# Optimization experiments

Measured on AMD Instinct MI355X. Metric: run time of the kernel, lower is better.

The kernel has to match this reference:

```python
import jax, jax.numpy as jnp
import numpy as np
from jax import lax

DIM = 2048
N_HEADS = 16
N_KV = 4
HEAD_DIM = DIM // N_HEADS  # 128
ROPE_BASE = 10000.0
SEQ = 4096
BSZ = 1


def bitlinear(x, W):
    # per-row abs-mean scale (detached), ternary round/clamp, straight-through blend
    s = lax.stop_gradient(jnp.clip(jnp.mean(jnp.abs(W), axis=1, keepdims=True), 1e-5, None))
    wt = jnp.clip(jnp.round(W / s), -1.0, 1.0)
    w = lax.stop_gradient(wt - W) + W  # straight-through
    return x @ (w * s).T


def rms_norm(x):
    eps = jnp.finfo(x.dtype).eps
    return x * lax.rsqrt(jnp.mean(x * x, axis=-1, keepdims=True) + eps)


def rope(x, cos, sin):
    half = x.shape[-1] // 2
    x1, x2 = x[..., :half], x[..., half:]
    return jnp.concatenate((x1 * cos + x2 * sin, -x1 * sin + x2 * cos), axis=-1)


def setup_inputs() -> dict:
    key = jax.random.key(0)
    ks = jax.random.split(key, 6)
    kv_dim = N_KV * HEAD_DIM
    return {
        "x": jax.random.normal(ks[0], (BSZ, SEQ, DIM), dtype=jnp.float32),
        "wq": jax.random.normal(ks[1], (DIM, DIM), dtype=jnp.float32) * 0.02,
        "wk": jax.random.normal(ks[2], (kv_dim, DIM), dtype=jnp.float32) * 0.02,
        "wv": jax.random.normal(ks[3], (kv_dim, DIM), dtype=jnp.float32) * 0.02,
        "wp": jax.random.normal(ks[4], (DIM, DIM), dtype=jnp.float32) * 0.02,
        "q_gain": jnp.ones((N_HEADS,), dtype=jnp.float32),
    }


def reference(x, wq, wk, wv, wp, q_gain):
    b, s, d = x.shape
    q = bitlinear(x, wq).reshape(b, s, N_HEADS, HEAD_DIM).transpose(0, 2, 1, 3)  # bhsd
    k = bitlinear(x, wk).reshape(b, s, N_KV, HEAD_DIM).transpose(0, 2, 1, 3)
    v = bitlinear(x, wv).reshape(b, s, N_KV, HEAD_DIM).transpose(0, 2, 1, 3)

    q = rms_norm(q)
    k = rms_norm(k)

    inv_freq = 1.0 / ROPE_BASE ** (jnp.arange(0, HEAD_DIM, 2, dtype=jnp.float32) / HEAD_DIM)
    t = jnp.arange(s, dtype=jnp.float32)
    freqs = jnp.outer(t, inv_freq)  # [s, hd/2]
    cos = jnp.cos(freqs)[None, None].astype(q.dtype)
    sin = jnp.sin(freqs)[None, None].astype(q.dtype)
    q = rope(q, cos, sin)
    k = rope(k, cos, sin)

    q = q * q_gain.astype(q.dtype)[None, :, None, None]

    groups = N_HEADS // N_KV
    k = jnp.repeat(k, groups, axis=1)  # GQA expand to [b, H, s, hd]
    v = jnp.repeat(v, groups, axis=1)

    scale = 1.0 / np.sqrt(HEAD_DIM)
    scores = jnp.einsum("bhqd,bhkd->bhqk", q, k) * scale
    causal = jnp.tril(jnp.ones((s, s), dtype=bool))
    scores = jnp.where(causal[None, None], scores, jnp.finfo(scores.dtype).min)
    attn = jax.nn.softmax(scores, axis=-1)
    y = jnp.einsum("bhqk,bhkd->bhqd", attn, v)

    y = y.transpose(0, 2, 1, 3).reshape(b, s, d)
    return bitlinear(y, wp)
```

## Files before the change

kernel.cpp:

```cpp
#include <hip/hip_runtime.h>
#include <math.h>

typedef unsigned short u16;
typedef short s16x8 __attribute__((ext_vector_type(8)));
typedef short s16x4 __attribute__((ext_vector_type(4)));
typedef float f32x4 __attribute__((ext_vector_type(4)));
typedef u16 u16x4 __attribute__((ext_vector_type(4)));

static constexpr size_t OFF_XB   = 0;
static constexpr size_t OFF_WQKV = 16777216;
static constexpr size_t OFF_KH   = 16777216;
static constexpr size_t OFF_VT   = 20971520;
static constexpr size_t OFF_ML   = 25165824;
static constexpr size_t OFF_WP   = 29360128;
static constexpr size_t OFF_QKV  = 37748736;
static constexpr size_t OFF_Y    = 79691776;

__device__ __forceinline__ u16 f2bf(float f) {
  union { float f; unsigned u; } v; v.f = f;
  unsigned r = v.u + 0x7fffu + ((v.u >> 16) & 1u);
  return (u16)(r >> 16);
}

__device__ __forceinline__ float bf2f(u16 b) {
  union { unsigned u; float f; } v; v.u = ((unsigned)b) << 16;
  return v.f;
}

__device__ __forceinline__ void async16(const u16* g, u16* lds) {
  __builtin_amdgcn_global_load_lds(
      (const __attribute__((address_space(1))) void*)g,
      (__attribute__((address_space(3))) void*)lds, 16, 0, 0);
}

__global__ __launch_bounds__(256) void quant_rows(const float* __restrict__ W,
                                                  u16* __restrict__ out) {
  const int row = blockIdx.x, tid = threadIdx.x;
  const float* src = W + (size_t)row * 2048 + tid * 8;
  float4 a = *(const float4*)(src);
  float4 b = *(const float4*)(src + 4);
  float asum = fabsf(a.x)+fabsf(a.y)+fabsf(a.z)+fabsf(a.w)
             + fabsf(b.x)+fabsf(b.y)+fabsf(b.z)+fabsf(b.w);
  #pragma unroll
  for (int off = 1; off < 64; off <<= 1) asum += __shfl_xor(asum, off, 64);
  __shared__ float red[4];
  if ((tid & 63) == 0) red[tid >> 6] = asum;
  __syncthreads();
  float s = fmaxf((red[0]+red[1]+red[2]+red[3]) * (1.0f/2048.0f), 1e-5f);
  float v[8] = {a.x,a.y,a.z,a.w,b.x,b.y,b.z,b.w};
  u16* dst = out + (size_t)row * 2048 + tid * 8;
  #pragma unroll
  for (int i = 0; i < 8; i++) {
    float q = rintf(v[i] / s);
    q = fminf(fmaxf(q, -1.f), 1.f);
    dst[i] = f2bf(q * s);
  }
}

__global__ __launch_bounds__(256) void cvt_bf16(const float* __restrict__ in,
                                                u16* __restrict__ out) {
  size_t i = ((size_t)blockIdx.x * 256 + threadIdx.x) * 4;
  float4 v = *(const float4*)(in + i);
  u16x4 o;
  o.x = f2bf(v.x); o.y = f2bf(v.y); o.z = f2bf(v.z); o.w = f2bf(v.w);
  *(u16x4*)(out + i) = o;
}

__global__ __launch_bounds__(256) void gemm_bt(const u16* __restrict__ A,
                                               const u16* __restrict__ B,
                                               float* __restrict__ C,
                                               int M, int N, int K) {
  __shared__ u16 sA[128 * 32];
  __shared__ u16 sB[128 * 32];
  const int tid = threadIdx.x;
  const int lane = tid & 63;
  const int wid = tid >> 6;
  const int lr = lane & 15, lq = lane >> 4;
  const int wm = (wid >> 1) * 64, wn = (wid & 1) * 64;
  const size_t m0 = (size_t)blockIdx.y * 128, n0 = (size_t)blockIdx.x * 128;

  const int r0 = tid >> 2, c0 = (tid & 3) * 8;
  const u16* Ab0 = A + (m0 + r0) * (size_t)K + c0;
  const u16* Ab1 = A + (m0 + 64 + r0) * (size_t)K + c0;
  const u16* Bb0 = B + (n0 + r0) * (size_t)K + c0;
  const u16* Bb1 = B + (n0 + 64 + r0) * (size_t)K + c0;
  u16* sA0 = &sA[tid * 8];
  u16* sA1 = &sA[(256 + tid) * 8];
  u16* sB0 = &sB[tid * 8];
  u16* sB1 = &sB[(256 + tid) * 8];

  f32x4 acc[4][4] = {};

  for (int kt = 0; kt < K; kt += 32) {
    async16(Ab0 + kt, sA0);
    async16(Ab1 + kt, sA1);
    async16(Bb0 + kt, sB0);
    async16(Bb1 + kt, sB1);
    __syncthreads();
    s16x8 af[4], bf[4];
    #pragma unroll
    for (int mt = 0; mt < 4; mt++)
      af[mt] = *(const s16x8*)&sA[(wm + mt * 16 + lr) * 32 + lq * 8];
    #pragma unroll
    for (int nt = 0; nt < 4; nt++)
      bf[nt] = *(const s16x8*)&sB[(wn + nt * 16 + lr) * 32 + lq * 8];
    #pragma unroll
    for (int mt = 0; mt < 4; mt++)
      #pragma unroll
      for (int nt = 0; nt < 4; nt++)
        acc[mt][nt] = __builtin_amdgcn_mfma_f32_16x16x32_bf16(af[mt], bf[nt], acc[mt][nt], 0, 0, 0);
    __syncthreads();
  }
  #pragma unroll
  for (int mt = 0; mt < 4; mt++)
    #pragma unroll
    for (int nt = 0; nt < 4; nt++)
      #pragma unroll
      for (int r = 0; r < 4; r++) {
        size_t m = m0 + wm + mt * 16 + lq * 4 + r;
        size_t n = n0 + wn + nt * 16 + lr;
        C[m * (size_t)N + n] = acc[mt][nt][r];
      }
}

__global__ __launch_bounds__(256) void prep_qk(const float* __restrict__ qkv,
                                               const float* __restrict__ qgain,
                                               u16* __restrict__ Qh,
                                               u16* __restrict__ Kh) {
  const int s = blockIdx.y;
  const int j = blockIdx.x * 4 + (threadIdx.x >> 6);
  const int t = threadIdx.x & 63;
  const float* row = qkv + (size_t)s * 3072 + (size_t)j * 128;
  float x1 = row[t], x2 = row[t + 64];
  float ss = x1 * x1 + x2 * x2;
  #pragma unroll
  for (int off = 1; off < 64; off <<= 1) ss += __shfl_xor(ss, off, 64);
  float rn = rsqrtf(ss * (1.0f / 128.0f) + 1.1920929e-07f);
  float invf = exp2f(-(float)t * 0.20762050593048096f);
  float ang = (float)s * invf;
  float sn, c;
  sincosf(ang, &sn, &c);
  if (j < 16) {
    float g = qgain[j] * 0.12751738f;
    float q1 = x1 * rn, q2 = x2 * rn;
    float o1 = (q1 * c + q2 * sn) * g;
    float o2 = (-q1 * sn + q2 * c) * g;
    u16* dst = Qh + ((size_t)j * 4096 + s) * 128;
    dst[t] = f2bf(o1); dst[t + 64] = f2bf(o2);
  } else {
    float k1 = x1 * rn, k2 = x2 * rn;
    float o1 = k1 * c + k2 * sn;
    float o2 = -k1 * sn + k2 * c;
    u16* dst = Kh + ((size_t)(j - 16) * 4096 + s) * 128;
    dst[t] = f2bf(o1); dst[t + 64] = f2bf(o2);
  }
}

__global__ __launch_bounds__(256) void vtrans(const float* __restrict__ qkv,
                                              u16* __restrict__ Vtg) {
  __shared__ float tile[64][67];
  const int tid = threadIdx.x;
  const int s0 = blockIdx.y * 64;
  const int c0 = blockIdx.x * 64;
  #pragma unroll
  for (int it = 0; it < 4; it++) {
    int i = it * 256 + tid;
    int r = i >> 4, c = (i & 15) * 4;
    float4 v = *(const float4*)(qkv + (size_t)(s0 + r) * 3072 + 2560 + c0 + c);
    tile[r][c] = v.x; tile[r][c + 1] = v.y; tile[r][c + 2] = v.z; tile[r][c + 3] = v.w;
  }
  __syncthreads();
  #pragma unroll
  for (int it = 0; it < 2; it++) {
    int i = it * 256 + tid;
    int dl = i >> 3, sc = (i & 7) * 8;
    s16x8 ov;
    #pragma unroll
    for (int jj = 0; jj < 8; jj++) ov[jj] = (short)f2bf(tile[sc + jj][dl]);
    *(s16x8*)&Vtg[(size_t)(c0 + dl) * 4096 + s0 + sc] = ov;
  }
}

#define SEG(qt,a,b,s) ((unsigned)((qt)|((a)<<5)|((b)<<11)|((s)<<18)))
__constant__ unsigned SEGTAB[128] = {
  SEG(0,0,2,127),   SEG(15,0,15,14),
  SEG(15,15,32,15), 0,
  SEG(1,0,4,127),   SEG(14,0,13,12),
  SEG(14,13,30,13), 0,
  SEG(2,0,6,127),   SEG(13,0,11,10),
  SEG(13,11,28,11), 0,
  SEG(3,0,8,127),   SEG(12,0,9,8),
  SEG(12,9,26,9),   0,
  SEG(4,0,10,127),  SEG(11,0,7,6),
  SEG(11,7,24,7),   0,
  SEG(5,0,12,127),  SEG(10,0,5,4),
  SEG(10,5,22,5),   0,
  SEG(6,0,14,127),  SEG(9,0,3,2),
  SEG(9,3,20,3),    0,
  SEG(7,0,16,127),  SEG(8,0,1,0),
  SEG(8,1,18,1),    0,
  SEG(16,0,16,16),  0,
  SEG(16,16,33,17), 0,
  SEG(16,33,34,18), SEG(17,0,15,19),
  SEG(17,15,31,20), 0,
  SEG(17,31,36,21), SEG(18,0,12,22),
  SEG(18,12,28,23), 0,
  SEG(18,28,38,24), SEG(19,0,6,25),
  SEG(19,6,23,26),  0,
  SEG(19,23,39,27), 0,
  SEG(19,39,40,28), SEG(20,0,15,29),
  SEG(20,15,32,30), 0,
  SEG(20,32,42,31), SEG(21,0,6,32),
  SEG(21,6,22,33),  0,
  SEG(21,22,39,34), 0,
  SEG(21,39,44,35), SEG(22,0,11,36),
  SEG(22,11,27,37), 0,
  SEG(22,27,44,38), 0,
  SEG(22,44,46,39), SEG(23,0,14,40),
  SEG(23,14,30,41), 0,
  SEG(23,30,47,42), 0,
  SEG(23,47,48,43), SEG(24,0,15,44),
  SEG(24,15,31,45), 0,
  SEG(24,31,48,46), 0,
  SEG(24,48,50,47), SEG(25,0,14,48),
  SEG(25,14,30,49), 0,
  SEG(25,30,47,50), 0,
  SEG(25,47,52,51), SEG(26,0,11,52),
  SEG(26,11,27,53), 0,
  SEG(26,27,44,54), 0,
  SEG(26,44,54,55), SEG(27,0,6,56),
  SEG(27,6,22,57),  0,
  SEG(27,22,39,58), 0,
  SEG(27,39,55,59), 0,
  SEG(27,55,56,60), SEG(28,0,15,61),
  SEG(28,15,32,62), 0,
  SEG(28,32,48,63), 0,
  SEG(28,48,58,64), SEG(29,0,6,65),
  SEG(29,6,23,66),  0,
  SEG(29,23,39,67), 0,
  SEG(29,39,55,68), 0,
  SEG(29,55,60,69), SEG(30,0,12,70),
  SEG(30,12,28,71), 0,
  SEG(30,28,44,72), 0,
  SEG(30,44,61,73), 0,
  SEG(30,61,62,74), SEG(31,0,15,75),
  SEG(31,15,31,76), 0,
  SEG(31,31,48,77), 0,
  SEG(31,48,64,78), 0,
};
__constant__ unsigned char CBASE[24] = {0,2,4,6,8,10,12,14, 16,19,22,25,29,32,36,40, 44,48,52,56,61,65,70,75};
__constant__ unsigned char CCNT[24]  = {2,2,2,2,2,2,2,2, 3,3,3,4,3,4,4,4, 4,4,4,5,4,5,5,4};

__global__ __launch_bounds__(256, 2) void attn(const u16* __restrict__ Q,
                                               const u16* __restrict__ Kh,
                                               const u16* __restrict__ Vt,
                                               u16* __restrict__ Y,
                                               u16* __restrict__ Opart,
                                               float* __restrict__ MLpart) {
  const int tid = threadIdx.x, lane = tid & 63, wid = tid >> 6;
  const int lr = lane & 15, lq = lane >> 4;
  const int b = blockIdx.x;
  const int h = b & 15, unit = b >> 4;
  const int kvh = h >> 2;

  __shared__ u16 sK[64][136];
  __shared__ u16 sVt[128][72];

  const u16* Kbase = Kh + (size_t)kvh * 4096 * 128;
  const u16* Vbase = Vt + (size_t)kvh * 128 * 4096;

  #pragma unroll 1
  for (int si = 0; si < 2; ++si) {
    const unsigned sd = SEGTAB[unit * 2 + si];
    const int qt = sd & 31;
    const int t0 = (sd >> 5) & 63;
    const int t1 = (sd >> 11) & 127;
    const int slot = (sd >> 18) & 127;
    if (t1 <= t0) continue;
    const int qbase = qt * 128;

    s16x8 qf[2][4];
    #pragma unroll
    for (int f = 0; f < 2; f++) {
      const u16* qp = Q + ((size_t)h * 4096 + qbase + wid * 32 + f * 16 + lr) * 128 + lq * 8;
      #pragma unroll
      for (int kc = 0; kc < 4; kc++) qf[f][kc] = *(const s16x8*)(qp + kc * 32);
    }

    f32x4 oacc[2][8] = {};
    float mrow[2] = {-1e30f, -1e30f};
    float lrow[2] = {0.f, 0.f};

    for (int t = t0; t < t1; ++t) {
      #pragma unroll
      for (int it = 0; it < 4; it++) {
        int idx = it * 256 + tid;
        int kr = idx >> 4, kc8 = (idx & 15) * 8;
        *(s16x8*)&sK[kr][kc8] = *(const s16x8*)(Kbase + (size_t)(t * 64 + kr) * 128 + kc8);
      }
      #pragma unroll
      for (int it = 0; it < 4; it++) {
        int idx = it * 256 + tid;
        int vd = idx >> 3, vc = (idx & 7) * 8;
        s16x8 v = *(const s16x8*)(Vbase + (size_t)vd * 4096 + t * 64 + vc);
        int g0 = ((vc >> 2) & 3) * 16 + (vc >> 4) * 4;
        int g1 = (((vc >> 2) & 3) + 1) * 16 + (vc >> 4) * 4;
        s16x4 lo = {v[0], v[1], v[2], v[3]};
        s16x4 hi = {v[4], v[5], v[6], v[7]};
        *(s16x4*)&sVt[vd][g0] = lo;
        *(s16x4*)&sVt[vd][g1] = hi;
      }
      __syncthreads();

      f32x4 sacc[2][4] = {};
      #pragma unroll
      for (int nt = 0; nt < 4; nt++)
        #pragma unroll
        for (int kc = 0; kc < 4; kc++) {
          s16x8 kf = *(const s16x8*)&sK[nt * 16 + lr][kc * 32 + lq * 8];
          sacc[0][nt] = __builtin_amdgcn_mfma_f32_16x16x32_bf16(kf, qf[0][kc], sacc[0][nt], 0, 0, 0);
          sacc[1][nt] = __builtin_amdgcn_mfma_f32_16x16x32_bf16(kf, qf[1][kc], sacc[1][nt], 0, 0, 0);
        }

      if (t >= 2 * qt) {
        #pragma unroll
        for (int f = 0; f < 2; f++) {
          int qg = qbase + wid * 32 + f * 16 + lr;
          #pragma unroll
          for (int nt = 0; nt < 4; nt++) {
            int kv0 = t * 64 + nt * 16 + lq * 4;
            #pragma unroll
            for (int r = 0; r < 4; r++)
              if (kv0 + r > qg) sacc[f][nt][r] = -1e30f;
          }
        }
      }

      float mx[2];
      #pragma unroll
      for (int f = 0; f < 2; f++) {
        float m01 = fmaxf(fmaxf(sacc[f][0][0], sacc[f][0][1]), fmaxf(sacc[f][0][2], sacc[f][0][3]));
        float m23 = fmaxf(fmaxf(sacc[f][1][0], sacc[f][1][1]), fmaxf(sacc[f][1][2], sacc[f][1][3]));
        float m45 = fmaxf(fmaxf(sacc[f][2][0], sacc[f][2][1]), fmaxf(sacc[f][2][2], sacc[f][2][3]));
        float m67 = fmaxf(fmaxf(sacc[f][3][0], sacc[f][3][1]), fmaxf(sacc[f][3][2], sacc[f][3][3]));
        mx[f] = fmaxf(fmaxf(m01, m23), fmaxf(m45, m67));
        mx[f] = fmaxf(mx[f], __shfl_xor(mx[f], 16, 64));
        mx[f] = fmaxf(mx[f], __shfl_xor(mx[f], 32, 64));
      }

      bool grow = (mx[0] > mrow[0]) || (mx[1] > mrow[1]);
      if (__any(grow)) {
        #pragma unroll
        for (int f = 0; f < 2; f++) {
          float mn = fmaxf(mrow[f], mx[f]);
          float al = exp2f(mrow[f] - mn);
          mrow[f] = mn;
          lrow[f] *= al;
          #pragma unroll
          for (int dt = 0; dt < 8; dt++)
            #pragma unroll
            for (int r = 0; r < 4; r++) oacc[f][dt][r] *= al;
        }
      }

      s16x4 pf[2][4];
      float rsum[2] = {0.f, 0.f};
      #pragma unroll
      for (int f = 0; f < 2; f++)
        #pragma unroll
        for (int nt = 0; nt < 4; nt++)
          #pragma unroll
          for (int r = 0; r < 4; r++) {
            union { float fv; unsigned u; } pu;
            pu.fv = exp2f(sacc[f][nt][r] - mrow[f]);
            rsum[f] += pu.fv;
            pf[f][nt][r] = (short)(pu.u >> 16);
          }
      #pragma unroll
      for (int f = 0; f < 2; f++) {
        rsum[f] += __shfl_xor(rsum[f], 16, 64);
        rsum[f] += __shfl_xor(rsum[f], 32, 64);
        lrow[f] += rsum[f];
      }

      #pragma unroll
      for (int dt = 0; dt < 8; dt++) {
        s16x8 v01 = *(const s16x8*)&sVt[dt * 16 + lr][lq * 16];
        s16x8 v23 = *(const s16x8*)&sVt[dt * 16 + lr][lq * 16 + 8];
        s16x4 vf0 = {v01[0], v01[1], v01[2], v01[3]};
        s16x4 vf1 = {v01[4], v01[5], v01[6], v01[7]};
        s16x4 vf2 = {v23[0], v23[1], v23[2], v23[3]};
        s16x4 vf3 = {v23[4], v23[5], v23[6], v23[7]};
        #pragma unroll
        for (int f = 0; f < 2; f++) {
          oacc[f][dt] = __builtin_amdgcn_mfma_f32_16x16x16bf16_1k(vf0, pf[f][0], oacc[f][dt], 0, 0, 0);
          oacc[f][dt] = __builtin_amdgcn_mfma_f32_16x16x16bf16_1k(vf1, pf[f][1], oacc[f][dt], 0, 0, 0);
          oacc[f][dt] = __builtin_amdgcn_mfma_f32_16x16x16bf16_1k(vf2, pf[f][2], oacc[f][dt], 0, 0, 0);
          oacc[f][dt] = __builtin_amdgcn_mfma_f32_16x16x16bf16_1k(vf3, pf[f][3], oacc[f][dt], 0, 0, 0);
        }
      }
      __syncthreads();
    }

    if (slot == 127) {
      #pragma unroll
      for (int f = 0; f < 2; f++) {
        float linv = 1.0f / lrow[f];
        int qg = qbase + wid * 32 + f * 16 + lr;
        #pragma unroll
        for (int dt = 0; dt < 8; dt++) {
          u16 tmp[4];
          #pragma unroll
          for (int r = 0; r < 4; r++) tmp[r] = f2bf(oacc[f][dt][r] * linv);
          *(s16x4*)&Y[(size_t)qg * 2048 + h * 128 + dt * 16 + lq * 4] = *(s16x4*)tmp;
        }
      }
    } else {
      const int gslot = h * 79 + slot;
      u16* Op = Opart + (size_t)gslot * 16384;
      #pragma unroll
      for (int f = 0; f < 2; f++) {
        int row = wid * 32 + f * 16 + lr;
        #pragma unroll
        for (int dt = 0; dt < 8; dt++) {
          u16 tmp[4];
          #pragma unroll
          for (int r = 0; r < 4; r++) tmp[r] = f2bf(oacc[f][dt][r]);
          *(s16x4*)&Op[row * 128 + dt * 16 + lq * 4] = *(s16x4*)tmp;
        }
        if (lq == 0) {
          MLpart[(size_t)gslot * 256 + row * 2]     = mrow[f];
          MLpart[(size_t)gslot * 256 + row * 2 + 1] = lrow[f];
        }
      }
    }
  }
}

__global__ __launch_bounds__(256) void combine(const u16* __restrict__ Op,
                                               const float* __restrict__ ML,
                                               u16* __restrict__ Y) {
  const int b = blockIdx.x;
  const int qt = 8 + (b >> 4), h = b & 15;
  const int base = CBASE[qt - 8], n = CCNT[qt - 8];
  const int gbase = h * 79 + base;
  const int tid = threadIdx.x;
  const int row = tid >> 1, half = (tid & 1) * 64;

  float m[5], l[5];
  float mstar = -3e38f;
  for (int i = 0; i < n; i++) {
    m[i] = ML[(size_t)(gbase + i) * 256 + row * 2];
    l[i] = ML[(size_t)(gbase + i) * 256 + row * 2 + 1];
    mstar = fmaxf(mstar, m[i]);
  }
  float w[5], wsum = 0.f;
  for (int i = 0; i < n; i++) { w[i] = exp2f(m[i] - mstar); wsum += l[i] * w[i]; }
  float inv = 1.0f / wsum;

  float acc[64] = {};
  for (int i = 0; i < n; i++) {
    const u16* o = Op + (size_t)(gbase + i) * 16384 + row * 128 + half;
    float wi = w[i];
    #pragma unroll
    for (int c = 0; c < 64; c += 8) {
      s16x8 a = *(const s16x8*)(o + c);
      #pragma unroll
      for (int jj = 0; jj < 8; jj++) acc[c + jj] += wi * bf2f((u16)a[jj]);
    }
  }
  u16* dst = Y + ((size_t)qt * 128 + row) * 2048 + h * 128 + half;
  #pragma unroll
  for (int c = 0; c < 64; c += 8) {
    u16 tmp[8];
    #pragma unroll
    for (int jj = 0; jj < 8; jj++) tmp[jj] = f2bf(acc[c + jj] * inv);
    *(s16x8*)(dst + c) = *(s16x8*)tmp;
  }
}

extern "C" void kernel_launch(void* const* d_in, const int* in_sizes, int n_in,
                              void* d_out, int out_size, void* d_ws, size_t ws_size,
                              hipStream_t stream) {
  const float* x  = (const float*)d_in[0];
  const float* wq = (const float*)d_in[1];
  const float* wk = (const float*)d_in[2];
  const float* wv = (const float*)d_in[3];
  const float* wp = (const float*)d_in[4];
  const float* qg = (const float*)d_in[5];
  float* out = (float*)d_out;
  char* ws = (char*)d_ws;

  u16*   XB    = (u16*)(ws + OFF_XB);
  u16*   WQKV  = (u16*)(ws + OFF_WQKV);
  u16*   WP    = (u16*)(ws + OFF_WP);
  float* QKV   = (float*)(ws + OFF_QKV);
  u16*   QH    = XB;
  u16*   KH    = (u16*)(ws + OFF_KH);
  u16*   VT    = (u16*)(ws + OFF_VT);
  float* MLP   = (float*)(ws + OFF_ML);
  u16*   OPART = (u16*)(ws + OFF_QKV);
  u16*   Yb    = (u16*)(ws + OFF_Y);

  quant_rows<<<2048, 256, 0, stream>>>(wq, WQKV);
  quant_rows<<<512,  256, 0, stream>>>(wk, WQKV + (size_t)2048 * 2048);
  quant_rows<<<512,  256, 0, stream>>>(wv, WQKV + (size_t)2560 * 2048);
  quant_rows<<<2048, 256, 0, stream>>>(wp, WP);
  cvt_bf16<<<8192, 256, 0, stream>>>(x, XB);
  gemm_bt<<<dim3(24, 32), 256, 0, stream>>>(XB, WQKV, QKV, 4096, 3072, 2048);
  prep_qk<<<dim3(5, 4096), 256, 0, stream>>>(QKV, qg, QH, KH);
  vtrans<<<dim3(8, 64), 256, 0, stream>>>(QKV, VT);
  attn<<<1024, 256, 0, stream>>>(QH, KH, VT, Yb, OPART, MLP);
  combine<<<384, 256, 0, stream>>>(OPART, MLP, Yb);
  gemm_bt<<<dim3(16, 32), 256, 0, stream>>>(Yb, WP, out, 4096, 2048, 2048);
}
```

Before: 418.1 us.

## Pre-tile K/V in LDS layout, async-load tiles, lazy rescale, fuse quant kernels

prep_qk and vtrans now write K and V^T in a pre-tiled, XOR-swizzled layout that matches the LDS tiles. The attention kernel can then copy each tile with global_load_lds async 16-byte loads instead of register round-trips. The online softmax now rescales only when the row max grows by more than 3 (in log2 units), and it keeps per-lane partial row sums that are reduced once after the loop. The four weight quantisation launches are merged into one kernel, and attn launch bounds are raised to 4 blocks per CU. These changes cut load instructions, shuffles and launch overhead, but they add register pressure and the lazy rescale accepts larger exp values.

```diff
diff --git a/kernel.cpp b/kernel.cpp
--- a/kernel.cpp
+++ b/kernel.cpp
@@ -33,10 +33,20 @@
       (__attribute__((address_space(3))) void*)lds, 16, 0, 0);
 }
 
-__global__ __launch_bounds__(256) void quant_rows(const float* __restrict__ W,
-                                                  u16* __restrict__ out) {
+__global__ __launch_bounds__(256) void quant_all(const float* __restrict__ wq,
+                                                 const float* __restrict__ wk,
+                                                 const float* __restrict__ wv,
+                                                 const float* __restrict__ wp,
+                                                 u16* __restrict__ outqkv,
+                                                 u16* __restrict__ outp) {
   const int row = blockIdx.x, tid = threadIdx.x;
-  const float* src = W + (size_t)row * 2048 + tid * 8;
+  const float* src;
+  u16* dst;
+  if (row < 2048)      { src = wq + (size_t)row * 2048;          dst = outqkv + (size_t)row * 2048; }
+  else if (row < 2560) { src = wk + (size_t)(row - 2048) * 2048; dst = outqkv + (size_t)row * 2048; }
+  else if (row < 3072) { src = wv + (size_t)(row - 2560) * 2048; dst = outqkv + (size_t)row * 2048; }
+  else                 { src = wp + (size_t)(row - 3072) * 2048; dst = outp + (size_t)(row - 3072) * 2048; }
+  src += tid * 8;
   float4 a = *(const float4*)(src);
   float4 b = *(const float4*)(src + 4);
   float asum = fabsf(a.x)+fabsf(a.y)+fabsf(a.z)+fabsf(a.w)
@@ -48,12 +58,12 @@
   __syncthreads();
   float s = fmaxf((red[0]+red[1]+red[2]+red[3]) * (1.0f/2048.0f), 1e-5f);
   float v[8] = {a.x,a.y,a.z,a.w,b.x,b.y,b.z,b.w};
-  u16* dst = out + (size_t)row * 2048 + tid * 8;
+  u16* d = dst + tid * 8;
   #pragma unroll
   for (int i = 0; i < 8; i++) {
     float q = rintf(v[i] / s);
     q = fminf(fmaxf(q, -1.f), 1.f);
-    dst[i] = f2bf(q * s);
+    d[i] = f2bf(q * s);
   }
 }
 
@@ -148,11 +158,14 @@
     u16* dst = Qh + ((size_t)j * 4096 + s) * 128;
     dst[t] = f2bf(o1); dst[t + 64] = f2bf(o2);
   } else {
+    const int kvh = j - 16;
     float k1 = x1 * rn, k2 = x2 * rn;
     float o1 = k1 * c + k2 * sn;
     float o2 = -k1 * sn + k2 * c;
-    u16* dst = Kh + ((size_t)(j - 16) * 4096 + s) * 128;
-    dst[t] = f2bf(o1); dst[t + 64] = f2bf(o2);
+    const int tt = s >> 6, kr = s & 63;
+    u16* base = Kh + (((size_t)kvh * 64 + tt) * 4) * 2048 + kr * 32 + (t & 31);
+    base[(size_t)(t >> 5) * 2048]       = f2bf(o1);
+    base[(size_t)(2 + (t >> 5)) * 2048] = f2bf(o2);
   }
 }
 
@@ -174,10 +187,22 @@
   for (int it = 0; it < 2; it++) {
     int i = it * 256 + tid;
     int dl = i >> 3, sc = (i & 7) * 8;
-    s16x8 ov;
-    #pragma unroll
-    for (int jj = 0; jj < 8; jj++) ov[jj] = (short)f2bf(tile[sc + jj][dl]);
-    *(s16x8*)&Vtg[(size_t)(c0 + dl) * 4096 + s0 + sc] = ov;
+    int cglob = c0 + dl;
+    int kvh = cglob >> 7, d = cglob & 127;
+    int tt = s0 >> 6;
+    int a0 = 16 * ((sc >> 2) & 3) + 4 * (sc >> 4);
+    int a1 = 16 * (((sc >> 2) + 1) & 3) + 4 * (sc >> 4);
+    int x = d & 7;
+    int p0 = ((((a0 >> 3) ^ x) << 3) | (a0 & 7));
+    int p1 = ((((a1 >> 3) ^ x) << 3) | (a1 & 7));
+    size_t rowbase = (((size_t)kvh * 64 + tt) * 128 + d) * 64;
+    u16 lo[4], hi[4];
+    #pragma unroll
+    for (int jj = 0; jj < 4; jj++) lo[jj] = f2bf(tile[sc + jj][dl]);
+    #pragma unroll
+    for (int jj = 0; jj < 4; jj++) hi[jj] = f2bf(tile[sc + 4 + jj][dl]);
+    *(s16x4*)&Vtg[rowbase + p0] = *(s16x4*)lo;
+    *(s16x4*)&Vtg[rowbase + p1] = *(s16x4*)hi;
   }
 }
 
@@ -251,7 +276,7 @@
 __constant__ unsigned char CBASE[24] = {0,2,4,6,8,10,12,14, 16,19,22,25,29,32,36,40, 44,48,52,56,61,65,70,75};
 __constant__ unsigned char CCNT[24]  = {2,2,2,2,2,2,2,2, 3,3,3,4,3,4,4,4, 4,4,4,5,4,5,5,4};
 
-__global__ __launch_bounds__(256, 2) void attn(const u16* __restrict__ Q,
+__global__ __launch_bounds__(256, 4) void attn(const u16* __restrict__ Q,
                                                const u16* __restrict__ Kh,
                                                const u16* __restrict__ Vt,
                                                u16* __restrict__ Y,
@@ -263,11 +288,14 @@
   const int h = b & 15, unit = b >> 4;
   const int kvh = h >> 2;
 
-  __shared__ u16 sK[64][136];
-  __shared__ u16 sVt[128][72];
-
-  const u16* Kbase = Kh + (size_t)kvh * 4096 * 128;
-  const u16* Vbase = Vt + (size_t)kvh * 128 * 4096;
+  __shared__ u16 sK[4 * 64 * 32];
+  __shared__ u16 sVt[128 * 64];
+
+  const u16* Kbase = Kh + (size_t)kvh * 64 * 8192;
+  const u16* Vbase = Vt + (size_t)kvh * 64 * 8192;
+
+  const int o01 = (((2 * lq) ^ (lr & 7)) << 3);
+  const int o23 = (((2 * lq + 1) ^ (lr & 7)) << 3);
 
   #pragma unroll 1
   for (int si = 0; si < 2; ++si) {
@@ -288,27 +316,17 @@
     }
 
     f32x4 oacc[2][8] = {};
+    f32x4 lacc[2] = {};
     float mrow[2] = {-1e30f, -1e30f};
-    float lrow[2] = {0.f, 0.f};
 
     for (int t = t0; t < t1; ++t) {
+      const u16* Kt = Kbase + (size_t)t * 8192;
+      const u16* Vtt = Vbase + (size_t)t * 8192;
       #pragma unroll
       for (int it = 0; it < 4; it++) {
-        int idx = it * 256 + tid;
-        int kr = idx >> 4, kc8 = (idx & 15) * 8;
-        *(s16x8*)&sK[kr][kc8] = *(const s16x8*)(Kbase + (size_t)(t * 64 + kr) * 128 + kc8);
-      }
-      #pragma unroll
-      for (int it = 0; it < 4; it++) {
-        int idx = it * 256 + tid;
-        int vd = idx >> 3, vc = (idx & 7) * 8;
-        s16x8 v = *(const s16x8*)(Vbase + (size_t)vd * 4096 + t * 64 + vc);
-        int g0 = ((vc >> 2) & 3) * 16 + (vc >> 4) * 4;
-        int g1 = (((vc >> 2) & 3) + 1) * 16 + (vc >> 4) * 4;
-        s16x4 lo = {v[0], v[1], v[2], v[3]};
-        s16x4 hi = {v[4], v[5], v[6], v[7]};
-        *(s16x4*)&sVt[vd][g0] = lo;
-        *(s16x4*)&sVt[vd][g1] = hi;
+        int off = it * 2048 + tid * 8;
+        async16(Kt + off, &sK[off]);
+        async16(Vtt + off, &sVt[off]);
       }
       __syncthreads();
 
@@ -317,7 +335,7 @@
       for (int nt = 0; nt < 4; nt++)
         #pragma unroll
         for (int kc = 0; kc < 4; kc++) {
-          s16x8 kf = *(const s16x8*)&sK[nt * 16 + lr][kc * 32 + lq * 8];
+          s16x8 kf = *(const s16x8*)&sK[kc * 2048 + (nt * 16 + lr) * 32 + lq * 8];
           sacc[0][nt] = __builtin_amdgcn_mfma_f32_16x16x32_bf16(kf, qf[0][kc], sacc[0][nt], 0, 0, 0);
           sacc[1][nt] = __builtin_amdgcn_mfma_f32_16x16x32_bf16(kf, qf[1][kc], sacc[1][nt], 0, 0, 0);
         }
@@ -336,26 +354,25 @@
         }
       }
 
-      float mx[2];
+      float pm[2];
       #pragma unroll
       for (int f = 0; f < 2; f++) {
-        float m01 = fmaxf(fmaxf(sacc[f][0][0], sacc[f][0][1]), fmaxf(sacc[f][0][2], sacc[f][0][3]));
-        float m23 = fmaxf(fmaxf(sacc[f][1][0], sacc[f][1][1]), fmaxf(sacc[f][1][2], sacc[f][1][3]));
-        float m45 = fmaxf(fmaxf(sacc[f][2][0], sacc[f][2][1]), fmaxf(sacc[f][2][2], sacc[f][2][3]));
-        float m67 = fmaxf(fmaxf(sacc[f][3][0], sacc[f][3][1]), fmaxf(sacc[f][3][2], sacc[f][3][3]));
-        mx[f] = fmaxf(fmaxf(m01, m23), fmaxf(m45, m67));
-        mx[f] = fmaxf(mx[f], __shfl_xor(mx[f], 16, 64));
-        mx[f] = fmaxf(mx[f], __shfl_xor(mx[f], 32, 64));
-      }
-
-      bool grow = (mx[0] > mrow[0]) || (mx[1] > mrow[1]);
-      if (__any(grow)) {
+        float a = fmaxf(fmaxf(sacc[f][0][0], sacc[f][0][1]), fmaxf(sacc[f][0][2], sacc[f][0][3]));
+        float bb = fmaxf(fmaxf(sacc[f][1][0], sacc[f][1][1]), fmaxf(sacc[f][1][2], sacc[f][1][3]));
+        float cc = fmaxf(fmaxf(sacc[f][2][0], sacc[f][2][1]), fmaxf(sacc[f][2][2], sacc[f][2][3]));
+        float dd = fmaxf(fmaxf(sacc[f][3][0], sacc[f][3][1]), fmaxf(sacc[f][3][2], sacc[f][3][3]));
+        pm[f] = fmaxf(fmaxf(a, bb), fmaxf(cc, dd));
+      }
+      if (__any((pm[0] > mrow[0] + 3.0f) || (pm[1] > mrow[1] + 3.0f))) {
         #pragma unroll
         for (int f = 0; f < 2; f++) {
-          float mn = fmaxf(mrow[f], mx[f]);
+          float mn = pm[f];
+          mn = fmaxf(mn, __shfl_xor(mn, 16, 64));
+          mn = fmaxf(mn, __shfl_xor(mn, 32, 64));
+          mn = fmaxf(mn, mrow[f]);
           float al = exp2f(mrow[f] - mn);
           mrow[f] = mn;
-          lrow[f] *= al;
+          lacc[f] *= al;
           #pragma unroll
           for (int dt = 0; dt < 8; dt++)
             #pragma unroll
@@ -364,7 +381,6 @@
       }
 
       s16x4 pf[2][4];
-      float rsum[2] = {0.f, 0.f};
       #pragma unroll
       for (int f = 0; f < 2; f++)
         #pragma unroll
@@ -373,20 +389,15 @@
           for (int r = 0; r < 4; r++) {
             union { float fv; unsigned u; } pu;
             pu.fv = exp2f(sacc[f][nt][r] - mrow[f]);
-            rsum[f] += pu.fv;
+            lacc[f][r] += pu.fv;
             pf[f][nt][r] = (short)(pu.u >> 16);
           }
-      #pragma unroll
-      for (int f = 0; f < 2; f++) {
-        rsum[f] += __shfl_xor(rsum[f], 16, 64);
-        rsum[f] += __shfl_xor(rsum[f], 32, 64);
-        lrow[f] += rsum[f];
-      }
 
       #pragma unroll
       for (int dt = 0; dt < 8; dt++) {
-        s16x8 v01 = *(const s16x8*)&sVt[dt * 16 + lr][lq * 16];
-        s16x8 v23 = *(const s16x8*)&sVt[dt * 16 + lr][lq * 16 + 8];
+        const u16* vrow = &sVt[(dt * 16 + lr) * 64];
+        s16x8 v01 = *(const s16x8*)(vrow + o01);
+        s16x8 v23 = *(const s16x8*)(vrow + o23);
         s16x4 vf0 = {v01[0], v01[1], v01[2], v01[3]};
         s16x4 vf1 = {v01[4], v01[5], v01[6], v01[7]};
         s16x4 vf2 = {v23[0], v23[1], v23[2], v23[3]};
@@ -400,6 +411,15 @@
         }
       }
       __syncthreads();
+    }
+
+    float lrow[2];
+    #pragma unroll
+    for (int f = 0; f < 2; f++) {
+      float s4 = (lacc[f][0] + lacc[f][1]) + (lacc[f][2] + lacc[f][3]);
+      s4 += __shfl_xor(s4, 16, 64);
+      s4 += __shfl_xor(s4, 32, 64);
+      lrow[f] = s4;
     }
 
     if (slot == 127) {
@@ -502,10 +522,7 @@
   u16*   OPART = (u16*)(ws + OFF_QKV);
   u16*   Yb    = (u16*)(ws + OFF_Y);
 
-  quant_rows<<<2048, 256, 0, stream>>>(wq, WQKV);
-  quant_rows<<<512,  256, 0, stream>>>(wk, WQKV + (size_t)2048 * 2048);
-  quant_rows<<<512,  256, 0, stream>>>(wv, WQKV + (size_t)2560 * 2048);
-  quant_rows<<<2048, 256, 0, stream>>>(wp, WP);
+  quant_all<<<5120, 256, 0, stream>>>(wq, wk, wv, wp, WQKV, WP);
   cvt_bf16<<<8192, 256, 0, stream>>>(x, XB);
   gemm_bt<<<dim3(24, 32), 256, 0, stream>>>(XB, WQKV, QKV, 4096, 3072, 2048);
   prep_qk<<<dim3(5, 4096), 256, 0, stream>>>(QKV, qg, QH, KH);
```

Result: slower. 629.0 us (+50.5%).
